# Kernel optimization log

Measured on AMD Instinct MI355X. Metric: run time of the kernel, lower is better.

Reference implementation:

```python
import jax, jax.numpy as jnp
import numpy as np

N_CLASSES = 40
EMBED_DIM = 128
MOMENTUM = 0.1
LAMBDA_R, LAMBDA_C, LAMBDA_M = 1.0, 0.5, 1.0
BATCH = 262144


def setup_inputs() -> dict:
    key = jax.random.key(0)
    k1, k2, k3 = jax.random.split(key, 3)
    z = jax.random.normal(k1, (BATCH, EMBED_DIM), dtype=jnp.float32)
    y = jax.random.randint(k2, (BATCH,), 0, N_CLASSES)
    centers = jax.random.normal(k3, (N_CLASSES, EMBED_DIM), dtype=jnp.float32)
    initialized = jnp.ones((N_CLASSES,), dtype=bool)
    # buffers derived from class_counts (imbalanced ramp), r0=gamma=m0=1, alpha=0.25
    counts = jnp.asarray([1000.0 * (i + 1) for i in range(N_CLASSES)], jnp.float32)
    n_max = jnp.max(counts)
    target_radii = 1.0 + 1.0 * jnp.log(n_max / (counts + 1.0))
    margins = 1.0 * jnp.power(n_max / (counts + 1.0), 0.25)
    return {"z": z, "y": y, "centers": centers, "initialized": initialized,
            "target_radii": target_radii, "margins": margins}


def _update_centers(z, y, centers, initialized):
    # EMA centroid update on detached embeddings (torch.no_grad equivalent).
    zs = jax.lax.stop_gradient(z)
    sums = jax.ops.segment_sum(zs, y, num_segments=N_CLASSES)            # [C, D]
    cnt = jax.ops.segment_sum(jnp.ones((zs.shape[0],), zs.dtype), y,
                              num_segments=N_CLASSES)                    # [C]
    mean = sums / jnp.maximum(cnt, 1.0)[:, None]
    ema = (1.0 - MOMENTUM) * centers + MOMENTUM * mean
    new = jnp.where(initialized[:, None], ema, mean)                     # first-touch init
    return jnp.where((cnt > 0)[:, None], new, centers)                   # skip empty classes


def reference(z, y, centers, initialized, target_radii, margins):
    c = _update_centers(z, y, centers, initialized)                      # [C, D]

    # radial loss: smooth L1 (beta=1) between ||z|| and per-class target radius
    r = jnp.linalg.norm(z, axis=-1)                                      # [B]
    d = r - target_radii[y]
    ad = jnp.abs(d)
    loss_radial = jnp.mean(jnp.where(ad < 1.0, 0.5 * d * d, ad - 0.5))

    # compact loss: mean squared distance to own centroid
    diff = z - c[y]                                                      # [B, D]
    loss_compact = jnp.mean(jnp.sum(diff * diff, axis=-1))

    # margin loss: min distance to any other class centroid via Gram trick
    z2 = jnp.sum(z * z, axis=-1)                                         # [B]
    c2 = jnp.sum(c * c, axis=-1)                                         # [C]
    d2 = z2[:, None] + c2[None, :] - 2.0 * (z @ c.T)                     # [B, C]
    dist = jnp.sqrt(jnp.maximum(d2, 0.0))
    own = y[:, None] == jnp.arange(N_CLASSES)[None, :]                   # [B, C] bool
    dist_opp = jnp.min(jnp.where(own, jnp.inf, dist), axis=1)            # [B]
    loss_margin = jnp.mean(jax.nn.relu(margins[y] - dist_opp))

    return LAMBDA_R * loss_radial + LAMBDA_C * loss_compact + LAMBDA_M * loss_margin
```

## Files before the change

### kernel.cpp

```cpp
#include <hip/hip_runtime.h>
#include <math.h>

#define BATCH 262144
#define DIM   128
#define NCLS  40
#define CD    (NCLS * DIM)

#define TB1 512
#define NB1 256
#define TB3 256
#define NB3 1024

__global__ __launch_bounds__(TB1) void k1_segsum(const float* __restrict__ z,
                                                 const int* __restrict__ y,
                                                 float* __restrict__ part_sums,
                                                 float* __restrict__ gcnt) {
    __shared__ float s_acc[8][NCLS * 64];
    __shared__ float s_cnt[NCLS];
    const int t = threadIdx.x;
    for (int i = t; i < 8 * NCLS * 64; i += TB1) ((float*)s_acc)[i] = 0.0f;
    if (t < NCLS) s_cnt[t] = 0.0f;
    __syncthreads();

    const int w    = t >> 6;
    const int lane = t & 63;
    const int p    = w >> 1;
    const int h    = w & 1;
    const int base = blockIdx.x * 1024;
    float* __restrict__ acc = s_acc[w];

    int yy[4];
#pragma unroll
    for (int g = 0; g < 4; ++g) yy[g] = y[base + 4 * (g * 64 + lane) + p];

    if (h == 0) {
#pragma unroll
        for (int g = 0; g < 4; ++g) atomicAdd(&s_cnt[yy[g]], 1.0f);
    }

    const float* __restrict__ zp = z + (size_t)base * DIM + h * 64 + lane;

    float vb[8];
#pragma unroll
    for (int q = 0; q < 8; ++q) vb[q] = zp[(size_t)(4 * q + p) * DIM];

#pragma unroll 1
    for (int g = 0; g < 4; ++g) {
        const int yg = yy[g];
#pragma unroll
        for (int j0 = 0; j0 < 64; j0 += 8) {
#pragma unroll
            for (int q = 0; q < 8; ++q) {
                const int sj = g * 64 + j0 + q;
                const float v = vb[q];
                int sn = sj + 8;
                if (sn > 255) sn = sj;
                vb[q] = zp[(size_t)(4 * sn + p) * DIM];
                const int cls = __builtin_amdgcn_readlane(yg, j0 + q);
                acc[cls * 64 + lane] += v;
            }
        }
    }
    __syncthreads();

    float* __restrict__ ps = part_sums + (size_t)blockIdx.x * CD;
    for (int i = t; i < CD; i += TB1) {
        const int cls = i >> 7;
        const int d   = i & 127;
        const int hh  = d >> 6, dl = d & 63;
        float ssum = 0.0f;
#pragma unroll
        for (int pp = 0; pp < 4; ++pp) ssum += s_acc[(pp << 1) | hh][cls * 64 + dl];
        ps[i] = ssum;
    }
    if (t < NCLS) atomicAdd(&gcnt[t], s_cnt[t]);
}

__global__ __launch_bounds__(DIM) void k2_centers(const float* __restrict__ part_sums,
                                                  const float* __restrict__ gcnt,
                                                  const float* __restrict__ centers,
                                                  float* __restrict__ c_out,
                                                  float* __restrict__ c2_out) {
    const int j = blockIdx.x;
    const int d = threadIdx.x;

    const float* __restrict__ p = part_sums + j * DIM + d;
    float s = 0.0f;
#pragma unroll 8
    for (int b = 0; b < NB1; ++b) s += p[(size_t)b * CD];
    const float cnt = gcnt[j];

    const float mean = s / fmaxf(cnt, 1.0f);
    const float ctr  = centers[j * DIM + d];
    const float ema  = 0.9f * ctr + 0.1f * mean;
    const float cv   = (cnt > 0.0f) ? ema : ctr;
    c_out[j * DIM + d] = cv;

    __shared__ float red[DIM];
    red[d] = cv * cv;
    __syncthreads();
    for (int off = DIM / 2; off > 0; off >>= 1) {
        if (d < off) red[d] += red[d + off];
        __syncthreads();
    }
    if (d == 0) c2_out[j] = red[0];
}

__global__ __launch_bounds__(TB3) void k3_loss(const float* __restrict__ z,
                                               const int* __restrict__ y,
                                               const float* __restrict__ cbuf,
                                               const float* __restrict__ c2,
                                               const float* __restrict__ tr,
                                               const float* __restrict__ mg,
                                               float* __restrict__ partials) {
    __shared__ float s_c[CD];
    __shared__ float s_c2[NCLS];
    {
        float4* d4 = (float4*)s_c;
        const float4* s4 = (const float4*)cbuf;
#pragma unroll
        for (int i = 0; i < 5; ++i) d4[i * TB3 + threadIdx.x] = s4[i * TB3 + threadIdx.x];
        if (threadIdx.x < NCLS) s_c2[threadIdx.x] = c2[threadIdx.x];
    }
    __syncthreads();

    const int row = blockIdx.x * TB3 + threadIdx.x;
    const float4* __restrict__ z4 = (const float4*)z + (size_t)row * 32;

    float4 zr[32];
#pragma unroll
    for (int k = 0; k < 32; ++k) zr[k] = z4[k];

    const int cls = y[row];

    float a0 = 0.f, a1 = 0.f, a2 = 0.f, a3 = 0.f;
#pragma unroll
    for (int k = 0; k < 32; ++k) {
        a0 = fmaf(zr[k].x, zr[k].x, a0);
        a1 = fmaf(zr[k].y, zr[k].y, a1);
        a2 = fmaf(zr[k].z, zr[k].z, a2);
        a3 = fmaf(zr[k].w, zr[k].w, a3);
    }
    const float z2 = (a0 + a1) + (a2 + a3);

    const float4* __restrict__ c4 = (const float4*)s_c;
    float own_d2 = 0.0f;
    float mind2  = 3.4e38f;
#pragma unroll 1
    for (int j = 0; j < NCLS; ++j) {
        float b0 = 0.f, b1 = 0.f, b2 = 0.f, b3 = 0.f;
#pragma unroll
        for (int k = 0; k < 32; ++k) {
            const float4 cv = c4[j * 32 + k];
            b0 = fmaf(zr[k].x, cv.x, b0);
            b1 = fmaf(zr[k].y, cv.y, b1);
            b2 = fmaf(zr[k].z, cv.z, b2);
            b3 = fmaf(zr[k].w, cv.w, b3);
        }
        const float dot = (b0 + b1) + (b2 + b3);
        const float d2  = z2 + s_c2[j] - 2.0f * dot;
        own_d2 = (j == cls) ? d2 : own_d2;
        mind2  = (j == cls) ? mind2 : fminf(mind2, d2);
    }

    const float r  = sqrtf(z2);
    const float dd = r - tr[cls];
    const float ad = fabsf(dd);
    const float rad = (ad < 1.0f) ? 0.5f * dd * dd : ad - 0.5f;

    const float dist = sqrtf(fmaxf(mind2, 0.0f));
    const float marg = fmaxf(mg[cls] - dist, 0.0f);

    float tot = rad + 0.5f * own_d2 + marg;

    __shared__ float sred[TB3];
    sred[threadIdx.x] = tot;
    __syncthreads();
    for (int off = TB3 / 2; off > 0; off >>= 1) {
        if (threadIdx.x < off) sred[threadIdx.x] += sred[threadIdx.x + off];
        __syncthreads();
    }
    if (threadIdx.x == 0) partials[blockIdx.x] = sred[0];
}

__global__ __launch_bounds__(256) void k4_final(const float* __restrict__ partials,
                                                float* __restrict__ out) {
    __shared__ float sred[256];
    float s = 0.0f;
    for (int i = threadIdx.x; i < NB3; i += 256) s += partials[i];
    sred[threadIdx.x] = s;
    __syncthreads();
    for (int off = 128; off > 0; off >>= 1) {
        if (threadIdx.x < off) sred[threadIdx.x] += sred[threadIdx.x + off];
        __syncthreads();
    }
    if (threadIdx.x == 0) out[0] = sred[0] * (1.0f / (float)BATCH);
}

extern "C" void kernel_launch(void* const* d_in, const int* in_sizes, int n_in,
                              void* d_out, int out_size, void* d_ws, size_t ws_size,
                              hipStream_t stream) {
    const float* z       = (const float*)d_in[0];
    const int*   y       = (const int*)d_in[1];
    const float* centers = (const float*)d_in[2];
    const float* tr      = (const float*)d_in[4];
    const float* mg      = (const float*)d_in[5];
    float* out = (float*)d_out;

    float* ws        = (float*)d_ws;
    float* part_sums = ws;
    float* cbuf      = part_sums + (size_t)NB1 * CD;
    float* c2buf     = cbuf + CD;
    float* gcnt      = c2buf + NCLS;
    float* partials  = gcnt + NCLS;

    hipMemsetAsync(gcnt, 0, NCLS * sizeof(float), stream);

    k1_segsum<<<NB1, TB1, 0, stream>>>(z, y, part_sums, gcnt);
    k2_centers<<<NCLS, DIM, 0, stream>>>(part_sums, gcnt, centers, cbuf, c2buf);
    k3_loss<<<NB3, TB3, 0, stream>>>(z, y, cbuf, c2buf, tr, mg, partials);
    k4_final<<<1, 256, 0, stream>>>(partials, out);
}
```

Measured before the change: 275.6 us.

## Compute z·c Gram products with bf16 MFMA instead of scalar FMA loop

The loss kernel now converts each z row and the updated centers to bf16 and computes the 40-class dot products with 16x16x32 bf16 MFMA instructions, padding the class count to 48 with dummy centers whose squared norm is huge. Results go through LDS so each thread can finish the per-row min-distance and loss scalar work. This replaces the per-thread 128x40 FP32 FMA loop, which kept a whole row in registers, with matrix-core work and fewer live registers. The cost is bf16 rounding in the distance computation, including the compact term derived from the Gram trick, which could shift the loss numerically.

```diff
diff --git a/kernel.cpp b/kernel.cpp
--- a/kernel.cpp
+++ b/kernel.cpp
@@ -4,12 +4,22 @@
 #define BATCH 262144
 #define DIM   128
 #define NCLS  40
+#define NCP   48
 #define CD    (NCLS * DIM)
 
 #define TB1 512
 #define NB1 256
 #define TB3 256
-#define NB3 1024
+#define NB3 (BATCH / 256)
+
+typedef __attribute__((ext_vector_type(8))) short short8;
+typedef __attribute__((ext_vector_type(4))) float f32x4;
+
+__device__ __forceinline__ short f2bf(float f) {
+    unsigned u = __float_as_uint(f);
+    u += 0x7fffu + ((u >> 16) & 1u);
+    return (short)(u >> 16);
+}
 
 __global__ __launch_bounds__(TB1) void k1_segsum(const float* __restrict__ z,
                                                  const int* __restrict__ y,
@@ -79,10 +89,16 @@
 __global__ __launch_bounds__(DIM) void k2_centers(const float* __restrict__ part_sums,
                                                   const float* __restrict__ gcnt,
                                                   const float* __restrict__ centers,
-                                                  float* __restrict__ c_out,
+                                                  short* __restrict__ cbf,
                                                   float* __restrict__ c2_out) {
     const int j = blockIdx.x;
     const int d = threadIdx.x;
+
+    if (j >= NCLS) {
+        cbf[j * DIM + d] = 0;
+        if (d == 0) c2_out[j] = 1e30f;
+        return;
+    }
 
     const float* __restrict__ p = part_sums + j * DIM + d;
     float s = 0.0f;
@@ -94,7 +110,7 @@
     const float ctr  = centers[j * DIM + d];
     const float ema  = 0.9f * ctr + 0.1f * mean;
     const float cv   = (cnt > 0.0f) ? ema : ctr;
-    c_out[j * DIM + d] = cv;
+    cbf[j * DIM + d] = f2bf(cv);
 
     __shared__ float red[DIM];
     red[d] = cv * cv;
@@ -108,79 +124,125 @@
 
 __global__ __launch_bounds__(TB3) void k3_loss(const float* __restrict__ z,
                                                const int* __restrict__ y,
-                                               const float* __restrict__ cbuf,
+                                               const short* __restrict__ cbf,
                                                const float* __restrict__ c2,
                                                const float* __restrict__ tr,
                                                const float* __restrict__ mg,
                                                float* __restrict__ partials) {
-    __shared__ float s_c[CD];
-    __shared__ float s_c2[NCLS];
-    {
-        float4* d4 = (float4*)s_c;
-        const float4* s4 = (const float4*)cbuf;
-#pragma unroll
-        for (int i = 0; i < 5; ++i) d4[i * TB3 + threadIdx.x] = s4[i * TB3 + threadIdx.x];
-        if (threadIdx.x < NCLS) s_c2[threadIdx.x] = c2[threadIdx.x];
-    }
-    __syncthreads();
-
-    const int row = blockIdx.x * TB3 + threadIdx.x;
-    const float4* __restrict__ z4 = (const float4*)z + (size_t)row * 32;
-
-    float4 zr[32];
-#pragma unroll
-    for (int k = 0; k < 32; ++k) zr[k] = z4[k];
-
+    __shared__ float s_S[4][64 * 52];
+    __shared__ float s_z2[4][64];
+    __shared__ float s_c2[NCP];
+    __shared__ float s_red[TB3];
+
+    const int t = threadIdx.x;
+    if (t < NCP) s_c2[t] = c2[t];
+
+    const int w    = t >> 6;
+    const int lane = t & 63;
+    const int q    = lane >> 4;
+    const int col  = lane & 15;
+    const int wavebase = blockIdx.x * 256 + w * 64;
+
+    short8 bfrag[3][4];
+#pragma unroll
+    for (int ct = 0; ct < 3; ++ct)
+#pragma unroll
+        for (int s = 0; s < 4; ++s)
+            bfrag[ct][s] = *(const short8*)(cbf + (ct * 16 + col) * DIM + s * 32 + q * 8);
+
+    __syncthreads();
+
+#pragma unroll 1
+    for (int rt = 0; rt < 4; ++rt) {
+        const float* __restrict__ zrow =
+            z + (size_t)(wavebase + rt * 16 + col) * DIM + q * 8;
+
+        float4 f[8];
+#pragma unroll
+        for (int s = 0; s < 4; ++s) {
+            f[2 * s]     = *(const float4*)(zrow + s * 32);
+            f[2 * s + 1] = *(const float4*)(zrow + s * 32 + 4);
+        }
+
+        float zp = 0.0f;
+#pragma unroll
+        for (int i = 0; i < 8; ++i) {
+            zp = fmaf(f[i].x, f[i].x, zp);
+            zp = fmaf(f[i].y, f[i].y, zp);
+            zp = fmaf(f[i].z, f[i].z, zp);
+            zp = fmaf(f[i].w, f[i].w, zp);
+        }
+
+        short8 afr[4];
+#pragma unroll
+        for (int s = 0; s < 4; ++s) {
+            const float4 f0 = f[2 * s], f1 = f[2 * s + 1];
+            afr[s][0] = f2bf(f0.x); afr[s][1] = f2bf(f0.y);
+            afr[s][2] = f2bf(f0.z); afr[s][3] = f2bf(f0.w);
+            afr[s][4] = f2bf(f1.x); afr[s][5] = f2bf(f1.y);
+            afr[s][6] = f2bf(f1.z); afr[s][7] = f2bf(f1.w);
+        }
+
+        f32x4 acc0 = {0.f, 0.f, 0.f, 0.f};
+        f32x4 acc1 = {0.f, 0.f, 0.f, 0.f};
+        f32x4 acc2 = {0.f, 0.f, 0.f, 0.f};
+#pragma unroll
+        for (int s = 0; s < 4; ++s) {
+            acc0 = __builtin_amdgcn_mfma_f32_16x16x32_bf16(afr[s], bfrag[0][s], acc0, 0, 0, 0);
+            acc1 = __builtin_amdgcn_mfma_f32_16x16x32_bf16(afr[s], bfrag[1][s], acc1, 0, 0, 0);
+            acc2 = __builtin_amdgcn_mfma_f32_16x16x32_bf16(afr[s], bfrag[2][s], acc2, 0, 0, 0);
+        }
+
+        zp += __shfl_xor(zp, 16);
+        zp += __shfl_xor(zp, 32);
+        if (q == 0) s_z2[w][rt * 16 + col] = zp;
+
+#pragma unroll
+        for (int reg = 0; reg < 4; ++reg) {
+            const int rr = rt * 16 + q * 4 + reg;
+            s_S[w][rr * 52 + col]      = acc0[reg];
+            s_S[w][rr * 52 + 16 + col] = acc1[reg];
+            s_S[w][rr * 52 + 32 + col] = acc2[reg];
+        }
+    }
+
+    const int row = blockIdx.x * 256 + t;
     const int cls = y[row];
-
-    float a0 = 0.f, a1 = 0.f, a2 = 0.f, a3 = 0.f;
-#pragma unroll
-    for (int k = 0; k < 32; ++k) {
-        a0 = fmaf(zr[k].x, zr[k].x, a0);
-        a1 = fmaf(zr[k].y, zr[k].y, a1);
-        a2 = fmaf(zr[k].z, zr[k].z, a2);
-        a3 = fmaf(zr[k].w, zr[k].w, a3);
-    }
-    const float z2 = (a0 + a1) + (a2 + a3);
-
-    const float4* __restrict__ c4 = (const float4*)s_c;
+    const float z2v = s_z2[w][lane];
+
     float own_d2 = 0.0f;
     float mind2  = 3.4e38f;
-#pragma unroll 1
-    for (int j = 0; j < NCLS; ++j) {
-        float b0 = 0.f, b1 = 0.f, b2 = 0.f, b3 = 0.f;
-#pragma unroll
-        for (int k = 0; k < 32; ++k) {
-            const float4 cv = c4[j * 32 + k];
-            b0 = fmaf(zr[k].x, cv.x, b0);
-            b1 = fmaf(zr[k].y, cv.y, b1);
-            b2 = fmaf(zr[k].z, cv.z, b2);
-            b3 = fmaf(zr[k].w, cv.w, b3);
-        }
-        const float dot = (b0 + b1) + (b2 + b3);
-        const float d2  = z2 + s_c2[j] - 2.0f * dot;
-        own_d2 = (j == cls) ? d2 : own_d2;
-        mind2  = (j == cls) ? mind2 : fminf(mind2, d2);
-    }
-
-    const float r  = sqrtf(z2);
+#pragma unroll
+    for (int k = 0; k < 12; ++k) {
+        const float4 Sv = *(const float4*)&s_S[w][lane * 52 + 4 * k];
+        const float Se[4] = {Sv.x, Sv.y, Sv.z, Sv.w};
+#pragma unroll
+        for (int e = 0; e < 4; ++e) {
+            const int j = 4 * k + e;
+            float d2 = fmaxf(z2v + s_c2[j] - 2.0f * Se[e], 0.0f);
+            const bool isown = (j == cls);
+            own_d2 = isown ? d2 : own_d2;
+            mind2  = isown ? mind2 : fminf(mind2, d2);
+        }
+    }
+
+    const float r  = sqrtf(z2v);
     const float dd = r - tr[cls];
     const float ad = fabsf(dd);
     const float rad = (ad < 1.0f) ? 0.5f * dd * dd : ad - 0.5f;
 
-    const float dist = sqrtf(fmaxf(mind2, 0.0f));
+    const float dist = sqrtf(mind2);
     const float marg = fmaxf(mg[cls] - dist, 0.0f);
 
-    float tot = rad + 0.5f * own_d2 + marg;
-
-    __shared__ float sred[TB3];
-    sred[threadIdx.x] = tot;
+    const float tot = rad + 0.5f * own_d2 + marg;
+
+    s_red[t] = tot;
     __syncthreads();
     for (int off = TB3 / 2; off > 0; off >>= 1) {
-        if (threadIdx.x < off) sred[threadIdx.x] += sred[threadIdx.x + off];
+        if (t < off) s_red[t] += s_red[t + off];
         __syncthreads();
     }
-    if (threadIdx.x == 0) partials[blockIdx.x] = sred[0];
+    if (t == 0) partials[blockIdx.x] = s_red[0];
 }
 
 __global__ __launch_bounds__(256) void k4_final(const float* __restrict__ partials,
@@ -209,15 +271,15 @@
 
     float* ws        = (float*)d_ws;
     float* part_sums = ws;
-    float* cbuf      = part_sums + (size_t)NB1 * CD;
-    float* c2buf     = cbuf + CD;
-    float* gcnt      = c2buf + NCLS;
+    float* c2buf     = part_sums + (size_t)NB1 * CD;
+    float* gcnt      = c2buf + NCP;
     float* partials  = gcnt + NCLS;
+    short* cbf       = (short*)(partials + NB3);
 
     hipMemsetAsync(gcnt, 0, NCLS * sizeof(float), stream);
 
     k1_segsum<<<NB1, TB1, 0, stream>>>(z, y, part_sums, gcnt);
-    k2_centers<<<NCLS, DIM, 0, stream>>>(part_sums, gcnt, centers, cbuf, c2buf);
-    k3_loss<<<NB3, TB3, 0, stream>>>(z, y, cbuf, c2buf, tr, mg, partials);
+    k2_centers<<<NCP, DIM, 0, stream>>>(part_sums, gcnt, centers, cbf, c2buf);
+    k3_loss<<<NB3, TB3, 0, stream>>>(z, y, cbf, c2buf, tr, mg, partials);
     k4_final<<<1, 256, 0, stream>>>(partials, out);
 }
```

Result: faster. 245.2 us (-11.0%).
